# Kernel optimization log

Measured on AMD Instinct MI355X. Metric: run time of the kernel, lower is better.

The kernel has to match this reference:

```python
import jax, jax.numpy as jnp
import numpy as np

B, N, D = 16, 4096, 768   # bags, instances per bag, feature dim
H, L, K = 12, 2, 16       # heads, MHA layers, topk
DH = D // H               # head dim (also gate hidden dim)


def _ln(x, g, b, eps=1e-5):
    m = x.mean(-1, keepdims=True)
    v = x.var(-1, keepdims=True)
    return (x - m) / jnp.sqrt(v + eps) * g + b


def setup_inputs() -> dict:
    key = jax.random.key(0)
    ks = jax.random.split(key, 8)
    s = 0.02
    return {
        "x": jax.random.normal(ks[0], (B, N, D), jnp.float32),
        "cls_token": jax.random.normal(ks[1], (1, 1, D), jnp.float32),
        "ln_g": jnp.ones((D,), jnp.float32),
        "ln_b": jnp.zeros((D,), jnp.float32),
        "gln_g": jnp.ones((D,), jnp.float32),
        "gln_b": jnp.zeros((D,), jnp.float32),
        "gW1": jax.random.normal(ks[2], (DH, D), jnp.float32) * s,
        "gb1": jnp.zeros((DH,), jnp.float32),
        "gW2": jax.random.normal(ks[3], (1, DH), jnp.float32) * s,
        "gb2": jnp.zeros((1,), jnp.float32),
        "Wqkv": jax.random.normal(ks[4], (L, 3 * D, D), jnp.float32) * s,
        "bqkv": jnp.zeros((L, 3 * D), jnp.float32),
        "Wo": jax.random.normal(ks[5], (L, D, D), jnp.float32) * s,
        "bo": jnp.zeros((L, D), jnp.float32),
    }


def reference(x, cls_token, ln_g, ln_b, gln_g, gln_b, gW1, gb1, gW2, gb2, Wqkv, bqkv, Wo, bo):
    # --- per-bag attention gate: LN -> Linear(D,DH) -> GELU -> Linear(DH,1) -> sigmoid ---
    z = _ln(x, gln_g, gln_b)                                      # [B,N,D]
    h = jax.nn.gelu(jnp.einsum('bnd,ed->bne', z, gW1) + gb1, approximate=False)
    w = jax.nn.sigmoid((jnp.einsum('bne,oe->bno', h, gW2) + gb2)[..., 0])  # [B,N]
    # --- top-k selection (argsort descending, take first K) + gather + weight ---
    topv, topi = jax.lax.top_k(w, K)                              # [B,K]
    sel = jnp.take_along_axis(x, topi[..., None], axis=1) * topv[..., None]  # [B,K,D]
    # --- prepend cls token, shared LayerNorm ---
    cls = jnp.broadcast_to(cls_token, (B, 1, D))
    seq = jnp.concatenate([cls, sel], axis=1)                     # [B,K+1,D]
    z0 = _ln(seq, ln_g, ln_b)
    a = z0
    S = K + 1
    scale = 1.0 / jnp.sqrt(jnp.asarray(DH, jnp.float32))
    # --- stacked MHA; residual always from z0, shared ln (matches source) ---
    for l in range(L):
        qkv = jnp.einsum('bsd,ed->bse', a, Wqkv[l]) + bqkv[l]     # [B,S,3D]
        q, k, v = jnp.split(qkv, 3, axis=-1)
        q = q.reshape(B, S, H, DH)
        k = k.reshape(B, S, H, DH)
        v = v.reshape(B, S, H, DH)
        att = jax.nn.softmax(jnp.einsum('bqhd,bkhd->bhqk', q, k) * scale, axis=-1)
        o = jnp.einsum('bhqk,bkhd->bqhd', att, v).reshape(B, S, D)
        o = jnp.einsum('bsd,ed->bse', o, Wo[l]) + bo[l]
        a = _ln(z0 + o, ln_g, ln_b)
    # dropout is identity in eval mode
    return a[:, 0, :]                                             # [B,D]
```

## Files before the change

kernel.cpp:

```cpp
#include <hip/hip_runtime.h>
#include <hip/hip_bf16.h>
#include <hip/hip_cooperative_groups.h>
#include <math.h>

namespace cg = cooperative_groups;

#define B_   16
#define N_   4096
#define D_   768
#define H_   12
#define L_   2
#define K_   16
#define S_   17
#define M_   272
#define BN_  65536
#define GRID_ 256

typedef __bf16 bf16x8 __attribute__((ext_vector_type(8)));
typedef float  f32x4  __attribute__((ext_vector_type(4)));

static __device__ __forceinline__ unsigned short f2bf(float f) {
    __bf16 h = (__bf16)f;
    return __builtin_bit_cast(unsigned short, h);
}
static __device__ __forceinline__ float bf2f(unsigned short u) {
    __bf16 h = __builtin_bit_cast(__bf16, u);
    return (float)h;
}
static __device__ __forceinline__ unsigned long long umax64(unsigned long long a, unsigned long long b) {
    return a > b ? a : b;
}


static __device__ __forceinline__
void gate_block(unsigned short* smem,
                const float* __restrict__ x,  const float* __restrict__ gln_g,
                const float* __restrict__ gln_b, const float* __restrict__ gW1,
                const float* __restrict__ gb1, const float* __restrict__ gW2,
                const float* __restrict__ gb2, float* __restrict__ wbuf,
                int bn0, int t)
{
    char* XhB = (char*)(smem);
    char* XlB = (char*)(smem + 8192);
    char* WhB = (char*)(smem + 16384);
    char* WlB = (char*)(smem + 20480);

    const int trow  = t >> 1;
    const int thalf = (t & 1) * 32;
    const int te    = t >> 2;
    const int tq    = (t & 3) * 16;

    const float* xrow = x + (size_t)(bn0 + trow) * D_ + thalf;
    const float* wrow = gW1 + (size_t)te * D_ + tq;

    const int wv = t >> 6;
    const int la = t & 63;
    const int fr = la & 15;
    const int fq = la >> 4;

    f32x4 acc[2][4];
    #pragma unroll
    for (int mi = 0; mi < 2; ++mi)
        #pragma unroll
        for (int ni = 0; ni < 4; ++ni) {
            f32x4 z = {0.f, 0.f, 0.f, 0.f};
            acc[mi][ni] = z;
        }

    float sxp = 0.f, sxxp = 0.f;
    float a1p = 0.f, a2p = 0.f;

    for (int kt = 0; kt < 12; ++kt) {
        __syncthreads();
        const float* src = xrow + kt * 64;
        #pragma unroll
        for (int j = 0; j < 8; ++j) {
            float4 v = *(const float4*)(src + j * 4);
            sxp  += v.x + v.y + v.z + v.w;
            sxxp += v.x * v.x + v.y * v.y + v.z * v.z + v.w * v.w;
            ushort4 hh, ll;
            hh.x = f2bf(v.x); ll.x = f2bf(v.x - bf2f(hh.x));
            hh.y = f2bf(v.y); ll.y = f2bf(v.y - bf2f(hh.y));
            hh.z = f2bf(v.z); ll.z = f2bf(v.z - bf2f(hh.z));
            hh.w = f2bf(v.w); ll.w = f2bf(v.w - bf2f(hh.w));
            int byte = trow * 128 + (thalf + j * 4) * 2;
            int sw   = byte ^ ((trow & 7) << 4);
            *(ushort4*)(XhB + sw) = hh;
            *(ushort4*)(XlB + sw) = ll;
        }
        const float* wsrc = wrow + kt * 64;
        const float* gsrc = gln_g + kt * 64 + tq;
        const float* bsrc = gln_b + kt * 64 + tq;
        #pragma unroll
        for (int j = 0; j < 4; ++j) {
            float4 w4 = *(const float4*)(wsrc + j * 4);
            float4 g4 = *(const float4*)(gsrc + j * 4);
            float4 b4 = *(const float4*)(bsrc + j * 4);
            float4 wt;
            wt.x = w4.x * g4.x; wt.y = w4.y * g4.y;
            wt.z = w4.z * g4.z; wt.w = w4.w * g4.w;
            a1p += wt.x + wt.y + wt.z + wt.w;
            a2p += b4.x * w4.x + b4.y * w4.y + b4.z * w4.z + b4.w * w4.w;
            ushort4 hh, ll;
            hh.x = f2bf(wt.x); ll.x = f2bf(wt.x - bf2f(hh.x));
            hh.y = f2bf(wt.y); ll.y = f2bf(wt.y - bf2f(hh.y));
            hh.z = f2bf(wt.z); ll.z = f2bf(wt.z - bf2f(hh.z));
            hh.w = f2bf(wt.w); ll.w = f2bf(wt.w - bf2f(hh.w));
            int byte = te * 128 + (tq + j * 4) * 2;
            int sw   = byte ^ ((te & 7) << 4);
            *(ushort4*)(WhB + sw) = hh;
            *(ushort4*)(WlB + sw) = ll;
        }
        __syncthreads();
        #pragma unroll
        for (int ks = 0; ks < 2; ++ks) {
            int k0 = ks * 32 + fq * 8;
            bf16x8 ah[2], al[2], bh[4], bl[4];
            #pragma unroll
            for (int mi = 0; mi < 2; ++mi) {
                int r    = wv * 32 + mi * 16 + fr;
                int byte = (r * 128 + k0 * 2) ^ ((r & 7) << 4);
                ah[mi] = *(const bf16x8*)(XhB + byte);
                al[mi] = *(const bf16x8*)(XlB + byte);
            }
            #pragma unroll
            for (int ni = 0; ni < 4; ++ni) {
                int e    = ni * 16 + fr;
                int byte = (e * 128 + k0 * 2) ^ ((e & 7) << 4);
                bh[ni] = *(const bf16x8*)(WhB + byte);
                bl[ni] = *(const bf16x8*)(WlB + byte);
            }
            #pragma unroll
            for (int mi = 0; mi < 2; ++mi)
                #pragma unroll
                for (int ni = 0; ni < 4; ++ni) {
                    acc[mi][ni] = __builtin_amdgcn_mfma_f32_16x16x32_bf16(ah[mi], bh[ni], acc[mi][ni], 0, 0, 0);
                    acc[mi][ni] = __builtin_amdgcn_mfma_f32_16x16x32_bf16(ah[mi], bl[ni], acc[mi][ni], 0, 0, 0);
                    acc[mi][ni] = __builtin_amdgcn_mfma_f32_16x16x32_bf16(al[mi], bh[ni], acc[mi][ni], 0, 0, 0);
                }
        }
    }
    __syncthreads();

    float* F    = (float*)smem;
    float* mS   = F;
    float* rS   = F + 128;
    float* A1s  = F + 256;
    float* A2s  = F + 320;
    float* redS = F + 384;
    float* redQ = F + 640;
    float* rA1  = F + 896;
    float* rA2  = F + 1152;

    redS[trow * 2 + (t & 1)] = sxp;
    redQ[trow * 2 + (t & 1)] = sxxp;
    rA1[te * 4 + (t & 3)] = a1p;
    rA2[te * 4 + (t & 3)] = a2p;
    __syncthreads();
    if (t < 128) {
        float s = redS[t * 2] + redS[t * 2 + 1];
        float q = redQ[t * 2] + redQ[t * 2 + 1];
        float m = s * (1.0f / D_);
        mS[t] = m;
        rS[t] = rsqrtf(q * (1.0f / D_) - m * m + 1e-5f);
    }
    if (t < 64) {
        A1s[t] = rA1[t * 4] + rA1[t * 4 + 1] + rA1[t * 4 + 2] + rA1[t * 4 + 3];
        A2s[t] = rA2[t * 4] + rA2[t * 4 + 1] + rA2[t * 4 + 2] + rA2[t * 4 + 3];
    }
    __syncthreads();

    float w2v[4], a1v[4], a2b[4];
    #pragma unroll
    for (int ni = 0; ni < 4; ++ni) {
        int e = ni * 16 + fr;
        w2v[ni] = gW2[e];
        a1v[ni] = A1s[e];
        a2b[ni] = A2s[e] + gb1[e];
    }
    float gb2v = gb2[0];

    #pragma unroll
    for (int mi = 0; mi < 2; ++mi) {
        #pragma unroll
        for (int j = 0; j < 4; ++j) {
            int inst = wv * 32 + mi * 16 + fq * 4 + j;
            float m = mS[inst], rs = rS[inst];
            float tp = 0.f;
            #pragma unroll
            for (int ni = 0; ni < 4; ++ni) {
                float h  = rs * (acc[mi][ni][j] - m * a1v[ni]) + a2b[ni];
                float hg = 0.5f * h * (1.0f + erff(h * 0.70710678118654752f));
                tp = fmaf(hg, w2v[ni], tp);
            }
            tp += __shfl_xor(tp, 1);
            tp += __shfl_xor(tp, 2);
            tp += __shfl_xor(tp, 4);
            tp += __shfl_xor(tp, 8);
            if (fr == 0) wbuf[bn0 + inst] = 1.0f / (1.0f + expf(-(tp + gb2v)));
        }
    }
}

static __device__ __forceinline__
void topk_block(unsigned long long* SB, const float* __restrict__ wbuf,
                float* __restrict__ topv, int* __restrict__ topi, int b, int t)
{
    unsigned long long* wred   = SB;
    unsigned long long* winkey = SB + 8;
    const int la = t & 63, wid = t >> 6;

    unsigned long long key[16];
    #pragma unroll
    for (int j = 0; j < 16; ++j) {
        int i = t + 256 * j;
        float v = wbuf[(size_t)b * N_ + i];
        key[j] = ((unsigned long long)__float_as_uint(v) << 12) | (unsigned long long)(4095 - i);
    }
    for (int k = 0; k < K_; ++k) {
        unsigned long long kk = key[0];
        #pragma unroll
        for (int j = 1; j < 16; ++j) kk = umax64(kk, key[j]);
        #pragma unroll
        for (int o = 1; o < 64; o <<= 1) kk = umax64(kk, (unsigned long long)__shfl_xor(kk, o));
        if (la == 0) wred[wid] = kk;
        __syncthreads();
        if (t == 0) {
            unsigned long long m = umax64(umax64(wred[0], wred[1]), umax64(wred[2], wred[3]));
            *winkey = m;
            int wi = 4095 - (int)(m & 0xfffULL);
            topv[b * K_ + k] = __uint_as_float((unsigned int)(m >> 12));
            topi[b * K_ + k] = wi;
        }
        __syncthreads();
        unsigned long long m = *winkey;
        int wi = 4095 - (int)(m & 0xfffULL);
        #pragma unroll
        for (int j = 0; j < 16; ++j)
            if (wi == t + 256 * j) key[j] = 0ULL;
        __syncthreads();
    }
}

static __device__ __forceinline__
void build_row(float* sm, const float* __restrict__ x, const float* __restrict__ cls,
               const float* __restrict__ ln_g, const float* __restrict__ ln_b,
               const float* __restrict__ topv, const int* __restrict__ topi,
               float* __restrict__ z0, float* __restrict__ abuf, int r, int t)
{
    const int b = r / S_, s = r % S_;
    float v[3];
    if (s == 0) {
        #pragma unroll
        for (int p = 0; p < 3; ++p) v[p] = cls[t + 256 * p];
    } else {
        int   idx = topi[b * K_ + s - 1];
        float tv  = topv[b * K_ + s - 1];
        const float* row = &x[((size_t)b * N_ + idx) * D_];
        #pragma unroll
        for (int p = 0; p < 3; ++p) v[p] = row[t + 256 * p] * tv;
    }
    float sum = 0.f, ss = 0.f;
    #pragma unroll
    for (int p = 0; p < 3; ++p) { sum += v[p]; ss += v[p] * v[p]; }
    #pragma unroll
    for (int o = 32; o; o >>= 1) { sum += __shfl_down(sum, o); ss += __shfl_down(ss, o); }
    int wid = t >> 6, la = t & 63;
    if (la == 0) { sm[wid * 2] = sum; sm[wid * 2 + 1] = ss; }
    __syncthreads();
    sum = sm[0] + sm[2] + sm[4] + sm[6];
    ss  = sm[1] + sm[3] + sm[5] + sm[7];
    __syncthreads();
    float m = sum * (1.0f / D_), rstd = rsqrtf(ss * (1.0f / D_) - m * m + 1e-5f);
    #pragma unroll
    for (int p = 0; p < 3; ++p) {
        int d = t + 256 * p;
        float z = (v[p] - m) * rstd * ln_g[d] + ln_b[d];
        z0[(size_t)r * D_ + d]   = z;
        abuf[(size_t)r * D_ + d] = z;
    }
}

static __device__ __forceinline__
void gemm_stage(char* SB, const float* __restrict__ A, const float* __restrict__ W,
                const float* __restrict__ bias, float* __restrict__ C, int N,
                int m0, int n0, int t)
{
    char* AhB = SB;
    char* AlB = SB + 8192;
    char* WhB = SB + 16384;
    char* WlB = SB + 24576;

    const int sr = t >> 2;
    const int sc = (t & 3) * 16;
    const int gm = m0 + sr;
    const bool aok = (gm < M_);
    const float* asrc = A + (size_t)gm * D_ + sc;
    const float* wsrc = W + (size_t)(n0 + sr) * D_ + sc;

    const int wv = t >> 6, la = t & 63;
    const int fr = la & 15, fq = la >> 4;
    const int wm = (wv & 1) * 32, wn = (wv >> 1) * 32;

    f32x4 acc[2][2];
    #pragma unroll
    for (int mi = 0; mi < 2; ++mi)
        #pragma unroll
        for (int ni = 0; ni < 2; ++ni) {
            f32x4 z = {0.f, 0.f, 0.f, 0.f};
            acc[mi][ni] = z;
        }

    float4 pa[4], pw[4];
    #pragma unroll
    for (int q = 0; q < 4; ++q) {
        pa[q] = aok ? *(const float4*)(asrc + q * 4) : make_float4(0.f, 0.f, 0.f, 0.f);
        pw[q] = *(const float4*)(wsrc + q * 4);
    }

    const int abyte0 = sr * 128 + sc * 2;
    const int asw0   = (abyte0)      ^ ((sr & 7) << 4);
    const int asw1   = (abyte0 + 16) ^ ((sr & 7) << 4);

    for (int kt = 0; kt < 12; ++kt) {
        __syncthreads();
        {
            ushort4 hh[4], ll[4];
            #pragma unroll
            for (int q = 0; q < 4; ++q) {
                hh[q].x = f2bf(pa[q].x); ll[q].x = f2bf(pa[q].x - bf2f(hh[q].x));
                hh[q].y = f2bf(pa[q].y); ll[q].y = f2bf(pa[q].y - bf2f(hh[q].y));
                hh[q].z = f2bf(pa[q].z); ll[q].z = f2bf(pa[q].z - bf2f(hh[q].z));
                hh[q].w = f2bf(pa[q].w); ll[q].w = f2bf(pa[q].w - bf2f(hh[q].w));
            }
            *(ushort4*)(AhB + asw0)     = hh[0];
            *(ushort4*)(AhB + asw0 + 8) = hh[1];
            *(ushort4*)(AhB + asw1)     = hh[2];
            *(ushort4*)(AhB + asw1 + 8) = hh[3];
            *(ushort4*)(AlB + asw0)     = ll[0];
            *(ushort4*)(AlB + asw0 + 8) = ll[1];
            *(ushort4*)(AlB + asw1)     = ll[2];
            *(ushort4*)(AlB + asw1 + 8) = ll[3];
            #pragma unroll
            for (int q = 0; q < 4; ++q) {
                hh[q].x = f2bf(pw[q].x); ll[q].x = f2bf(pw[q].x - bf2f(hh[q].x));
                hh[q].y = f2bf(pw[q].y); ll[q].y = f2bf(pw[q].y - bf2f(hh[q].y));
                hh[q].z = f2bf(pw[q].z); ll[q].z = f2bf(pw[q].z - bf2f(hh[q].z));
                hh[q].w = f2bf(pw[q].w); ll[q].w = f2bf(pw[q].w - bf2f(hh[q].w));
            }
            *(ushort4*)(WhB + asw0)     = hh[0];
            *(ushort4*)(WhB + asw0 + 8) = hh[1];
            *(ushort4*)(WhB + asw1)     = hh[2];
            *(ushort4*)(WhB + asw1 + 8) = hh[3];
            *(ushort4*)(WlB + asw0)     = ll[0];
            *(ushort4*)(WlB + asw0 + 8) = ll[1];
            *(ushort4*)(WlB + asw1)     = ll[2];
            *(ushort4*)(WlB + asw1 + 8) = ll[3];
        }
        __syncthreads();
        if (kt < 11) {
            const float* an  = asrc + (kt + 1) * 64;
            const float* wn2 = wsrc + (kt + 1) * 64;
            #pragma unroll
            for (int q = 0; q < 4; ++q) {
                pa[q] = aok ? *(const float4*)(an + q * 4) : make_float4(0.f, 0.f, 0.f, 0.f);
                pw[q] = *(const float4*)(wn2 + q * 4);
            }
        }
        #pragma unroll
        for (int ks = 0; ks < 2; ++ks) {
            int kb = ks * 64 + fq * 16;
            bf16x8 ah[2], al[2], bh[2], bl[2];
            #pragma unroll
            for (int mi = 0; mi < 2; ++mi) {
                int r    = wm + mi * 16 + fr;
                int byte = (r * 128 + kb) ^ ((r & 7) << 4);
                ah[mi] = *(const bf16x8*)(AhB + byte);
                al[mi] = *(const bf16x8*)(AlB + byte);
            }
            #pragma unroll
            for (int ni = 0; ni < 2; ++ni) {
                int r    = wn + ni * 16 + fr;
                int byte = (r * 128 + kb) ^ ((r & 7) << 4);
                bh[ni] = *(const bf16x8*)(WhB + byte);
                bl[ni] = *(const bf16x8*)(WlB + byte);
            }
            #pragma unroll
            for (int mi = 0; mi < 2; ++mi)
                #pragma unroll
                for (int ni = 0; ni < 2; ++ni) {
                    acc[mi][ni] = __builtin_amdgcn_mfma_f32_16x16x32_bf16(ah[mi], bh[ni], acc[mi][ni], 0, 0, 0);
                    acc[mi][ni] = __builtin_amdgcn_mfma_f32_16x16x32_bf16(ah[mi], bl[ni], acc[mi][ni], 0, 0, 0);
                    acc[mi][ni] = __builtin_amdgcn_mfma_f32_16x16x32_bf16(al[mi], bh[ni], acc[mi][ni], 0, 0, 0);
                }
        }
    }

    #pragma unroll
    for (int mi = 0; mi < 2; ++mi) {
        #pragma unroll
        for (int j = 0; j < 4; ++j) {
            int m = m0 + wm + mi * 16 + fq * 4 + j;
            if (m < M_) {
                #pragma unroll
                for (int ni = 0; ni < 2; ++ni) {
                    int n = n0 + wn + ni * 16 + fr;
                    C[(size_t)m * N + n] = acc[mi][ni][j] + bias[n];
                }
            }
        }
    }
}

static __device__ __forceinline__
void attn_block(float* F, const float* __restrict__ qkvb, float* __restrict__ obuf,
                int bh, int t)
{
    float* qs  = F;
    float* ks  = F + S_ * 65;
    float* vs  = F + 2 * S_ * 65;
    float* att = F + 3 * S_ * 65;
    const int b = bh / H_, h = bh % H_;
    const int bq = b * S_;
    for (int idx = t; idx < S_ * 64; idx += 256) {
        int s = idx >> 6, d = idx & 63;
        size_t off = (size_t)(bq + s) * (3 * D_) + h * 64 + d;
        qs[s * 65 + d] = qkvb[off];
        ks[s * 65 + d] = qkvb[off + D_];
        vs[s * 65 + d] = qkvb[off + 2 * D_];
    }
    __syncthreads();
    for (int idx = t; idx < S_ * S_; idx += 256) {
        int i = idx / S_, j = idx % S_;
        float sdot = 0.f;
        #pragma unroll
        for (int d = 0; d < 64; ++d) sdot = fmaf(qs[i * 65 + d], ks[j * 65 + d], sdot);
        att[i * 18 + j] = sdot * 0.125f;
    }
    __syncthreads();
    if (t < S_) {
        float mx = -1e30f;
        for (int j = 0; j < S_; ++j) mx = fmaxf(mx, att[t * 18 + j]);
        float ssum = 0.f;
        for (int j = 0; j < S_; ++j) { float e = expf(att[t * 18 + j] - mx); att[t * 18 + j] = e; ssum += e; }
        float inv = 1.0f / ssum;
        for (int j = 0; j < S_; ++j) att[t * 18 + j] *= inv;
    }
    __syncthreads();
    for (int idx = t; idx < S_ * 64; idx += 256) {
        int i = idx >> 6, d = idx & 63;
        float s = 0.f;
        #pragma unroll
        for (int j = 0; j < S_; ++j) s = fmaf(att[i * 18 + j], vs[j * 65 + d], s);
        obuf[(size_t)(bq + i) * D_ + h * 64 + d] = s;
    }
}

static __device__ __forceinline__
void resln_row(float* sm, const float* __restrict__ z0, const float* __restrict__ projb,
               const float* __restrict__ ln_g, const float* __restrict__ ln_b,
               float* __restrict__ abuf, float* __restrict__ out, int r, int t, int writeOut)
{
    float v[3];
    #pragma unroll
    for (int p = 0; p < 3; ++p) {
        int d = t + 256 * p;
        v[p] = z0[(size_t)r * D_ + d] + projb[(size_t)r * D_ + d];
    }
    float sum = 0.f, ss = 0.f;
    #pragma unroll
    for (int p = 0; p < 3; ++p) { sum += v[p]; ss += v[p] * v[p]; }
    #pragma unroll
    for (int o = 32; o; o >>= 1) { sum += __shfl_down(sum, o); ss += __shfl_down(ss, o); }
    int wid = t >> 6, la = t & 63;
    if (la == 0) { sm[wid * 2] = sum; sm[wid * 2 + 1] = ss; }
    __syncthreads();
    sum = sm[0] + sm[2] + sm[4] + sm[6];
    ss  = sm[1] + sm[3] + sm[5] + sm[7];
    __syncthreads();
    float m = sum * (1.0f / D_), rstd = rsqrtf(ss * (1.0f / D_) - m * m + 1e-5f);
    #pragma unroll
    for (int p = 0; p < 3; ++p) {
        int d = t + 256 * p;
        float a = (v[p] - m) * rstd * ln_g[d] + ln_b[d];
        abuf[(size_t)r * D_ + d] = a;
        if (writeOut && (r % S_) == 0) out[(size_t)(r / S_) * D_ + d] = a;
    }
}

__global__ __launch_bounds__(256)
void fused_kernel(const float* __restrict__ x, const float* __restrict__ cls,
                  const float* __restrict__ ln_g, const float* __restrict__ ln_b,
                  const float* __restrict__ gln_g, const float* __restrict__ gln_b,
                  const float* __restrict__ gW1, const float* __restrict__ gb1,
                  const float* __restrict__ gW2, const float* __restrict__ gb2,
                  const float* __restrict__ Wqkv, const float* __restrict__ bqkv,
                  const float* __restrict__ Wo, const float* __restrict__ bo,
                  float* out,
                  float* wbuf, float* topv, int* topi,
                  float* z0, float* abuf, float* qkvb, float* obuf, float* projb)
{
    cg::grid_group grid = cg::this_grid();
    __shared__ __align__(16) char SMEM[49152];
    const int bid = blockIdx.x;
    const int t   = threadIdx.x;

    #pragma unroll 1
    for (int half = 0; half < 2; ++half)
        gate_block((unsigned short*)SMEM, x, gln_g, gln_b, gW1, gb1, gW2, gb2,
                   wbuf, bid * 256 + half * 128, t);
    grid.sync();

    if (bid < B_) topk_block((unsigned long long*)SMEM, wbuf, topv, topi, bid, t);
    grid.sync();

    #pragma unroll 1
    for (int r = bid; r < M_; r += GRID_)
        build_row((float*)SMEM, x, cls, ln_g, ln_b, topv, topi, z0, abuf, r, t);
    grid.sync();

    #pragma unroll 1
    for (int l = 0; l < L_; ++l) {
        if (bid < 180)
            gemm_stage(SMEM, abuf, Wqkv + (size_t)l * 3 * D_ * D_,
                       bqkv + (size_t)l * 3 * D_, qkvb, 3 * D_,
                       (bid / 36) * 64, (bid % 36) * 64, t);
        grid.sync();

        if (bid < B_ * H_) attn_block((float*)SMEM, qkvb, obuf, bid, t);
        grid.sync();

        if (bid < 60)
            gemm_stage(SMEM, obuf, Wo + (size_t)l * D_ * D_,
                       bo + (size_t)l * D_, projb, D_,
                       (bid / 12) * 64, (bid % 12) * 64, t);
        grid.sync();

        #pragma unroll 1
        for (int r = bid; r < M_; r += GRID_)
            resln_row((float*)SMEM, z0, projb, ln_g, ln_b, abuf, out, r, t,
                      (l == L_ - 1) ? 1 : 0);
        if (l == 0) grid.sync();
    }
}

__global__ __launch_bounds__(256)
void gate_kernel(const float* __restrict__ x, const float* __restrict__ gln_g,
                 const float* __restrict__ gln_b, const float* __restrict__ gW1,
                 const float* __restrict__ gb1, const float* __restrict__ gW2,
                 const float* __restrict__ gb2, float* __restrict__ wbuf)
{
    __shared__ __align__(16) unsigned short smem[24576];
    gate_block(smem, x, gln_g, gln_b, gW1, gb1, gW2, gb2, wbuf,
               blockIdx.x * 128, threadIdx.x);
}

__global__ __launch_bounds__(256)
void topk_kernel(const float* __restrict__ wbuf, float* __restrict__ topv,
                 int* __restrict__ topi)
{
    __shared__ unsigned long long SB[16];
    topk_block(SB, wbuf, topv, topi, blockIdx.x, threadIdx.x);
}

__global__ __launch_bounds__(256)
void build_kernel(const float* __restrict__ x, const float* __restrict__ cls,
                  const float* __restrict__ ln_g, const float* __restrict__ ln_b,
                  const float* __restrict__ topv, const int* __restrict__ topi,
                  float* __restrict__ z0, float* __restrict__ abuf)
{
    __shared__ float sm[8];
    build_row(sm, x, cls, ln_g, ln_b, topv, topi, z0, abuf, blockIdx.x, threadIdx.x);
}

__global__ __launch_bounds__(256)
void gemm_mfma(const float* __restrict__ A, const float* __restrict__ W,
               const float* __restrict__ bias, float* __restrict__ C, int N)
{
    __shared__ __align__(16) char SB[32768];
    gemm_stage(SB, A, W, bias, C, N, blockIdx.x * 64, blockIdx.y * 64, threadIdx.x);
}

__global__ __launch_bounds__(256)
void attn_kernel(const float* __restrict__ qkvb, float* __restrict__ obuf)
{
    __shared__ __align__(16) float F[3 * S_ * 65 + S_ * 18];
    attn_block(F, qkvb, obuf, blockIdx.x, threadIdx.x);
}

__global__ __launch_bounds__(256)
void resln_kernel(const float* __restrict__ z0, const float* __restrict__ projb,
                  const float* __restrict__ ln_g, const float* __restrict__ ln_b,
                  float* __restrict__ abuf, float* __restrict__ out, int writeOut)
{
    __shared__ float sm[8];
    resln_row(sm, z0, projb, ln_g, ln_b, abuf, out, blockIdx.x, threadIdx.x, writeOut);
}

extern "C" void kernel_launch(void* const* d_in, const int* in_sizes, int n_in,
                              void* d_out, int out_size, void* d_ws, size_t ws_size,
                              hipStream_t stream)
{
    const float* x     = (const float*)d_in[0];
    const float* cls   = (const float*)d_in[1];
    const float* ln_g  = (const float*)d_in[2];
    const float* ln_b  = (const float*)d_in[3];
    const float* gln_g = (const float*)d_in[4];
    const float* gln_b = (const float*)d_in[5];
    const float* gW1   = (const float*)d_in[6];
    const float* gb1   = (const float*)d_in[7];
    const float* gW2   = (const float*)d_in[8];
    const float* gb2   = (const float*)d_in[9];
    const float* Wqkv  = (const float*)d_in[10];
    const float* bqkv  = (const float*)d_in[11];
    const float* Wo    = (const float*)d_in[12];
    const float* bo    = (const float*)d_in[13];
    float* out = (float*)d_out;

    float* ws   = (float*)d_ws;
    float* wbuf = ws;
    float* topv = ws + BN_;
    int*   topi = (int*)(ws + BN_ + 256);
    float* z0   = ws + BN_ + 512;
    float* abuf = z0 + (size_t)M_ * D_;
    float* qkvb = abuf + (size_t)M_ * D_;
    float* obuf = qkvb + (size_t)M_ * 3 * D_;
    float* projb = obuf + (size_t)M_ * D_;

    hipError_t lerr = hipErrorUnknown;
    int nb = 0;
    if (hipOccupancyMaxActiveBlocksPerMultiprocessor(
            &nb, (const void*)fused_kernel, 256, 0) == hipSuccess && nb >= 1) {
        void* args[] = {
            (void*)&x, (void*)&cls, (void*)&ln_g, (void*)&ln_b,
            (void*)&gln_g, (void*)&gln_b, (void*)&gW1, (void*)&gb1,
            (void*)&gW2, (void*)&gb2, (void*)&Wqkv, (void*)&bqkv,
            (void*)&Wo, (void*)&bo, (void*)&out,
            (void*)&wbuf, (void*)&topv, (void*)&topi,
            (void*)&z0, (void*)&abuf, (void*)&qkvb, (void*)&obuf, (void*)&projb
        };
        lerr = hipLaunchCooperativeKernel((const void*)fused_kernel, dim3(GRID_),
                                          dim3(256), args, 0, stream);
    }
    if (lerr != hipSuccess) {
        gate_kernel<<<BN_ / 128, 256, 0, stream>>>(x, gln_g, gln_b, gW1, gb1, gW2, gb2, wbuf);
        topk_kernel<<<B_, 256, 0, stream>>>(wbuf, topv, topi);
        build_kernel<<<M_, 256, 0, stream>>>(x, cls, ln_g, ln_b, topv, topi, z0, abuf);
        for (int l = 0; l < L_; ++l) {
            gemm_mfma<<<dim3(5, 36), 256, 0, stream>>>(abuf, Wqkv + (size_t)l * 3 * D_ * D_,
                                                       bqkv + (size_t)l * 3 * D_, qkvb, 3 * D_);
            attn_kernel<<<B_ * H_, 256, 0, stream>>>(qkvb, obuf);
            gemm_mfma<<<dim3(5, 12), 256, 0, stream>>>(obuf, Wo + (size_t)l * D_ * D_,
                                                       bo + (size_t)l * D_, projb, D_);
            resln_kernel<<<M_, 256, 0, stream>>>(z0, projb, ln_g, ln_b, abuf, out,
                                                 (l == L_ - 1) ? 1 : 0);
        }
    }
}
```

Baseline: 180.4 us.

## Replace cooperative grid kernel with fused per-stage launches and per-head QKV+attention

Drops the cooperative single-kernel design with grid-wide syncs and goes back to separate kernel launches. Top-k is merged with row building, and each head's QKV projection is fused with its attention so the qkv buffer never goes to global memory. The final layer's LN runs only on the cls rows. This removes grid.sync overhead and some intermediate traffic, but adds launch overhead and recomputes A-tile splits once per head.

```diff
diff --git a/kernel.cpp b/kernel.cpp
--- a/kernel.cpp
+++ b/kernel.cpp
@@ -1,9 +1,6 @@
 #include <hip/hip_runtime.h>
 #include <hip/hip_bf16.h>
-#include <hip/hip_cooperative_groups.h>
 #include <math.h>
-
-namespace cg = cooperative_groups;
 
 #define B_   16
 #define N_   4096
@@ -14,7 +11,6 @@
 #define S_   17
 #define M_   272
 #define BN_  65536
-#define GRID_ 256
 
 typedef __bf16 bf16x8 __attribute__((ext_vector_type(8)));
 typedef float  f32x4  __attribute__((ext_vector_type(4)));
@@ -30,20 +26,27 @@
 static __device__ __forceinline__ unsigned long long umax64(unsigned long long a, unsigned long long b) {
     return a > b ? a : b;
 }
-
-
-static __device__ __forceinline__
-void gate_block(unsigned short* smem,
-                const float* __restrict__ x,  const float* __restrict__ gln_g,
-                const float* __restrict__ gln_b, const float* __restrict__ gW1,
-                const float* __restrict__ gb1, const float* __restrict__ gW2,
-                const float* __restrict__ gb2, float* __restrict__ wbuf,
-                int bn0, int t)
+static __device__ __forceinline__ void split4(const float4& v, ushort4& hh, ushort4& ll) {
+    hh.x = f2bf(v.x); ll.x = f2bf(v.x - bf2f(hh.x));
+    hh.y = f2bf(v.y); ll.y = f2bf(v.y - bf2f(hh.y));
+    hh.z = f2bf(v.z); ll.z = f2bf(v.z - bf2f(hh.z));
+    hh.w = f2bf(v.w); ll.w = f2bf(v.w - bf2f(hh.w));
+}
+
+__global__ __launch_bounds__(256)
+void gate_kernel(const float* __restrict__ x, const float* __restrict__ gln_g,
+                 const float* __restrict__ gln_b, const float* __restrict__ gW1,
+                 const float* __restrict__ gb1, const float* __restrict__ gW2,
+                 const float* __restrict__ gb2, float* __restrict__ wbuf)
 {
+    __shared__ __align__(16) unsigned short smem[24576];
     char* XhB = (char*)(smem);
     char* XlB = (char*)(smem + 8192);
     char* WhB = (char*)(smem + 16384);
     char* WlB = (char*)(smem + 20480);
+
+    const int t   = threadIdx.x;
+    const int bn0 = blockIdx.x * 128;
 
     const int trow  = t >> 1;
     const int thalf = (t & 1) * 32;
@@ -79,10 +82,7 @@
             sxp  += v.x + v.y + v.z + v.w;
             sxxp += v.x * v.x + v.y * v.y + v.z * v.z + v.w * v.w;
             ushort4 hh, ll;
-            hh.x = f2bf(v.x); ll.x = f2bf(v.x - bf2f(hh.x));
-            hh.y = f2bf(v.y); ll.y = f2bf(v.y - bf2f(hh.y));
-            hh.z = f2bf(v.z); ll.z = f2bf(v.z - bf2f(hh.z));
-            hh.w = f2bf(v.w); ll.w = f2bf(v.w - bf2f(hh.w));
+            split4(v, hh, ll);
             int byte = trow * 128 + (thalf + j * 4) * 2;
             int sw   = byte ^ ((trow & 7) << 4);
             *(ushort4*)(XhB + sw) = hh;
@@ -102,10 +102,7 @@
             a1p += wt.x + wt.y + wt.z + wt.w;
             a2p += b4.x * w4.x + b4.y * w4.y + b4.z * w4.z + b4.w * w4.w;
             ushort4 hh, ll;
-            hh.x = f2bf(wt.x); ll.x = f2bf(wt.x - bf2f(hh.x));
-            hh.y = f2bf(wt.y); ll.y = f2bf(wt.y - bf2f(hh.y));
-            hh.z = f2bf(wt.z); ll.z = f2bf(wt.z - bf2f(hh.z));
-            hh.w = f2bf(wt.w); ll.w = f2bf(wt.w - bf2f(hh.w));
+            split4(wt, hh, ll);
             int byte = te * 128 + (tq + j * 4) * 2;
             int sw   = byte ^ ((te & 7) << 4);
             *(ushort4*)(WhB + sw) = hh;
@@ -202,12 +199,14 @@
     }
 }
 
-static __device__ __forceinline__
-void topk_block(unsigned long long* SB, const float* __restrict__ wbuf,
-                float* __restrict__ topv, int* __restrict__ topi, int b, int t)
+__global__ __launch_bounds__(256)
+void topkbuild_kernel(const float* __restrict__ x, const float* __restrict__ cls,
+                      const float* __restrict__ ln_g, const float* __restrict__ ln_b,
+                      const float* __restrict__ wbuf, float* __restrict__ z0)
 {
-    unsigned long long* wred   = SB;
-    unsigned long long* winkey = SB + 8;
+    __shared__ unsigned long long SB[40];
+    __shared__ float sm[8];
+    const int b = blockIdx.x, t = threadIdx.x;
     const int la = t & 63, wid = t >> 6;
 
     unsigned long long key[16];
@@ -223,73 +222,199 @@
         for (int j = 1; j < 16; ++j) kk = umax64(kk, key[j]);
         #pragma unroll
         for (int o = 1; o < 64; o <<= 1) kk = umax64(kk, (unsigned long long)__shfl_xor(kk, o));
-        if (la == 0) wred[wid] = kk;
+        if (la == 0) SB[wid] = kk;
         __syncthreads();
         if (t == 0) {
-            unsigned long long m = umax64(umax64(wred[0], wred[1]), umax64(wred[2], wred[3]));
-            *winkey = m;
-            int wi = 4095 - (int)(m & 0xfffULL);
-            topv[b * K_ + k] = __uint_as_float((unsigned int)(m >> 12));
-            topi[b * K_ + k] = wi;
-        }
-        __syncthreads();
-        unsigned long long m = *winkey;
+            unsigned long long m = umax64(umax64(SB[0], SB[1]), umax64(SB[2], SB[3]));
+            SB[8] = m;
+            SB[16 + k] = m;
+        }
+        __syncthreads();
+        unsigned long long m = SB[8];
         int wi = 4095 - (int)(m & 0xfffULL);
         #pragma unroll
         for (int j = 0; j < 16; ++j)
             if (wi == t + 256 * j) key[j] = 0ULL;
         __syncthreads();
     }
-}
-
-static __device__ __forceinline__
-void build_row(float* sm, const float* __restrict__ x, const float* __restrict__ cls,
-               const float* __restrict__ ln_g, const float* __restrict__ ln_b,
-               const float* __restrict__ topv, const int* __restrict__ topi,
-               float* __restrict__ z0, float* __restrict__ abuf, int r, int t)
+
+    for (int s = 0; s < S_; ++s) {
+        float v[3];
+        if (s == 0) {
+            #pragma unroll
+            for (int p = 0; p < 3; ++p) v[p] = cls[t + 256 * p];
+        } else {
+            unsigned long long m = SB[16 + s - 1];
+            int   idx = 4095 - (int)(m & 0xfffULL);
+            float tv  = __uint_as_float((unsigned int)(m >> 12));
+            const float* row = &x[((size_t)b * N_ + idx) * D_];
+            #pragma unroll
+            for (int p = 0; p < 3; ++p) v[p] = row[t + 256 * p] * tv;
+        }
+        float sum = 0.f, ss = 0.f;
+        #pragma unroll
+        for (int p = 0; p < 3; ++p) { sum += v[p]; ss += v[p] * v[p]; }
+        #pragma unroll
+        for (int o = 32; o; o >>= 1) { sum += __shfl_down(sum, o); ss += __shfl_down(ss, o); }
+        if (la == 0) { sm[wid * 2] = sum; sm[wid * 2 + 1] = ss; }
+        __syncthreads();
+        sum = sm[0] + sm[2] + sm[4] + sm[6];
+        ss  = sm[1] + sm[3] + sm[5] + sm[7];
+        __syncthreads();
+        float m = sum * (1.0f / D_), rstd = rsqrtf(ss * (1.0f / D_) - m * m + 1e-5f);
+        #pragma unroll
+        for (int p = 0; p < 3; ++p) {
+            int d = t + 256 * p;
+            z0[((size_t)(b * S_ + s)) * D_ + d] = (v[p] - m) * rstd * ln_g[d] + ln_b[d];
+        }
+    }
+}
+
+__global__ __launch_bounds__(256)
+void qkvattn_kernel(const float* __restrict__ A, const float* __restrict__ Wq,
+                    const float* __restrict__ bq, float* __restrict__ obuf)
 {
-    const int b = r / S_, s = r % S_;
-    float v[3];
-    if (s == 0) {
-        #pragma unroll
-        for (int p = 0; p < 3; ++p) v[p] = cls[t + 256 * p];
-    } else {
-        int   idx = topi[b * K_ + s - 1];
-        float tv  = topv[b * K_ + s - 1];
-        const float* row = &x[((size_t)b * N_ + idx) * D_];
-        #pragma unroll
-        for (int p = 0; p < 3; ++p) v[p] = row[t + 256 * p] * tv;
-    }
-    float sum = 0.f, ss = 0.f;
-    #pragma unroll
-    for (int p = 0; p < 3; ++p) { sum += v[p]; ss += v[p] * v[p]; }
-    #pragma unroll
-    for (int o = 32; o; o >>= 1) { sum += __shfl_down(sum, o); ss += __shfl_down(ss, o); }
-    int wid = t >> 6, la = t & 63;
-    if (la == 0) { sm[wid * 2] = sum; sm[wid * 2 + 1] = ss; }
-    __syncthreads();
-    sum = sm[0] + sm[2] + sm[4] + sm[6];
-    ss  = sm[1] + sm[3] + sm[5] + sm[7];
-    __syncthreads();
-    float m = sum * (1.0f / D_), rstd = rsqrtf(ss * (1.0f / D_) - m * m + 1e-5f);
-    #pragma unroll
-    for (int p = 0; p < 3; ++p) {
-        int d = t + 256 * p;
-        float z = (v[p] - m) * rstd * ln_g[d] + ln_b[d];
-        z0[(size_t)r * D_ + d]   = z;
-        abuf[(size_t)r * D_ + d] = z;
-    }
-}
-
-static __device__ __forceinline__
-void gemm_stage(char* SB, const float* __restrict__ A, const float* __restrict__ W,
-                const float* __restrict__ bias, float* __restrict__ C, int N,
-                int m0, int n0, int t)
+    __shared__ __align__(16) char SMEM[57344];
+    char* AhB = SMEM;
+    char* AlB = SMEM + 4096;
+    char* WhB = SMEM + 8192;
+    char* WlB = SMEM + 32768;
+
+    const int bid = blockIdx.x, b = bid / H_, h = bid % H_;
+    const int t = threadIdx.x;
+    const int wv = t >> 6, la = t & 63, fr = la & 15, fq = la >> 4;
+
+    const int ar  = t >> 3;
+    const int ac  = (t & 7) * 8;
+    const int wr4 = t >> 2;
+    const int wc  = (t & 3) * 16;
+
+    f32x4 acc[2][3];
+    #pragma unroll
+    for (int mi = 0; mi < 2; ++mi)
+        #pragma unroll
+        for (int ni = 0; ni < 3; ++ni) {
+            f32x4 z = {0.f, 0.f, 0.f, 0.f};
+            acc[mi][ni] = z;
+        }
+
+    for (int kt = 0; kt < 12; ++kt) {
+        __syncthreads();
+        #pragma unroll
+        for (int q2 = 0; q2 < 2; ++q2) {
+            ushort4 hh = {0, 0, 0, 0}, ll = {0, 0, 0, 0};
+            if (ar < S_) {
+                float4 v = *(const float4*)(A + ((size_t)(b * S_ + ar)) * D_ + kt * 64 + ac + q2 * 4);
+                split4(v, hh, ll);
+            }
+            int byte = (ar * 128 + (ac + q2 * 4) * 2) ^ ((ar & 7) << 4);
+            *(ushort4*)(AhB + byte) = hh;
+            *(ushort4*)(AlB + byte) = ll;
+        }
+        #pragma unroll
+        for (int jj = 0; jj < 3; ++jj) {
+            int wr   = jj * 64 + wr4;
+            int grow = (wr >> 6) * D_ + h * 64 + (wr & 63);
+            const float* wsrc = Wq + (size_t)grow * D_ + kt * 64 + wc;
+            #pragma unroll
+            for (int q4 = 0; q4 < 4; ++q4) {
+                float4 w = *(const float4*)(wsrc + q4 * 4);
+                ushort4 hh, ll;
+                split4(w, hh, ll);
+                int byte = (wr * 128 + (wc + q4 * 4) * 2) ^ ((wr & 7) << 4);
+                *(ushort4*)(WhB + byte) = hh;
+                *(ushort4*)(WlB + byte) = ll;
+            }
+        }
+        __syncthreads();
+        #pragma unroll
+        for (int ks = 0; ks < 2; ++ks) {
+            int kb = ks * 64 + fq * 16;
+            bf16x8 ah[2], al[2], bh[3], bl[3];
+            #pragma unroll
+            for (int mi = 0; mi < 2; ++mi) {
+                int r    = mi * 16 + fr;
+                int byte = (r * 128 + kb) ^ ((r & 7) << 4);
+                ah[mi] = *(const bf16x8*)(AhB + byte);
+                al[mi] = *(const bf16x8*)(AlB + byte);
+            }
+            #pragma unroll
+            for (int ni = 0; ni < 3; ++ni) {
+                int r    = (wv * 3 + ni) * 16 + fr;
+                int byte = (r * 128 + kb) ^ ((r & 7) << 4);
+                bh[ni] = *(const bf16x8*)(WhB + byte);
+                bl[ni] = *(const bf16x8*)(WlB + byte);
+            }
+            #pragma unroll
+            for (int mi = 0; mi < 2; ++mi)
+                #pragma unroll
+                for (int ni = 0; ni < 3; ++ni) {
+                    acc[mi][ni] = __builtin_amdgcn_mfma_f32_16x16x32_bf16(ah[mi], bh[ni], acc[mi][ni], 0, 0, 0);
+                    acc[mi][ni] = __builtin_amdgcn_mfma_f32_16x16x32_bf16(ah[mi], bl[ni], acc[mi][ni], 0, 0, 0);
+                    acc[mi][ni] = __builtin_amdgcn_mfma_f32_16x16x32_bf16(al[mi], bh[ni], acc[mi][ni], 0, 0, 0);
+                }
+        }
+    }
+    __syncthreads();
+
+    float* QKV = (float*)SMEM;
+    float* att = (float*)(SMEM + S_ * 200 * 4);
+
+    #pragma unroll
+    for (int mi = 0; mi < 2; ++mi)
+        #pragma unroll
+        for (int j = 0; j < 4; ++j) {
+            int row = mi * 16 + fq * 4 + j;
+            if (row < S_) {
+                #pragma unroll
+                for (int ni = 0; ni < 3; ++ni) {
+                    int col  = (wv * 3 + ni) * 16 + fr;
+                    int grow = (col >> 6) * D_ + h * 64 + (col & 63);
+                    QKV[row * 200 + col] = acc[mi][ni][j] + bq[grow];
+                }
+            }
+        }
+    __syncthreads();
+
+    for (int idx = t; idx < S_ * S_; idx += 256) {
+        int i = idx / S_, j = idx % S_;
+        float sdot = 0.f;
+        #pragma unroll
+        for (int d = 0; d < 64; ++d)
+            sdot = fmaf(QKV[i * 200 + d], QKV[j * 200 + 64 + d], sdot);
+        att[i * 18 + j] = sdot * 0.125f;
+    }
+    __syncthreads();
+    if (t < S_) {
+        float mx = -1e30f;
+        for (int j = 0; j < S_; ++j) mx = fmaxf(mx, att[t * 18 + j]);
+        float ssum = 0.f;
+        for (int j = 0; j < S_; ++j) { float e = expf(att[t * 18 + j] - mx); att[t * 18 + j] = e; ssum += e; }
+        float inv = 1.0f / ssum;
+        for (int j = 0; j < S_; ++j) att[t * 18 + j] *= inv;
+    }
+    __syncthreads();
+    for (int idx = t; idx < S_ * 64; idx += 256) {
+        int i = idx >> 6, d = idx & 63;
+        float s = 0.f;
+        #pragma unroll
+        for (int j = 0; j < S_; ++j) s = fmaf(att[i * 18 + j], QKV[j * 200 + 128 + d], s);
+        obuf[((size_t)(b * S_ + i)) * D_ + h * 64 + d] = s;
+    }
+}
+
+__global__ __launch_bounds__(256)
+void gemm_mfma(const float* __restrict__ A, const float* __restrict__ W,
+               const float* __restrict__ bias, float* __restrict__ C, int N)
 {
+    __shared__ __align__(16) char SB[32768];
     char* AhB = SB;
     char* AlB = SB + 8192;
     char* WhB = SB + 16384;
     char* WlB = SB + 24576;
+
+    const int t  = threadIdx.x;
+    const int m0 = blockIdx.x * 64, n0 = blockIdx.y * 64;
 
     const int sr = t >> 2;
     const int sc = (t & 3) * 16;
@@ -327,12 +452,7 @@
         {
             ushort4 hh[4], ll[4];
             #pragma unroll
-            for (int q = 0; q < 4; ++q) {
-                hh[q].x = f2bf(pa[q].x); ll[q].x = f2bf(pa[q].x - bf2f(hh[q].x));
-                hh[q].y = f2bf(pa[q].y); ll[q].y = f2bf(pa[q].y - bf2f(hh[q].y));
-                hh[q].z = f2bf(pa[q].z); ll[q].z = f2bf(pa[q].z - bf2f(hh[q].z));
-                hh[q].w = f2bf(pa[q].w); ll[q].w = f2bf(pa[q].w - bf2f(hh[q].w));
-            }
+            for (int q = 0; q < 4; ++q) split4(pa[q], hh[q], ll[q]);
             *(ushort4*)(AhB + asw0)     = hh[0];
             *(ushort4*)(AhB + asw0 + 8) = hh[1];
             *(ushort4*)(AhB + asw1)     = hh[2];
@@ -342,12 +462,7 @@
             *(ushort4*)(AlB + asw1)     = ll[2];
             *(ushort4*)(AlB + asw1 + 8) = ll[3];
             #pragma unroll
-            for (int q = 0; q < 4; ++q) {
-                hh[q].x = f2bf(pw[q].x); ll[q].x = f2bf(pw[q].x - bf2f(hh[q].x));
-                hh[q].y = f2bf(pw[q].y); ll[q].y = f2bf(pw[q].y - bf2f(hh[q].y));
-                hh[q].z = f2bf(pw[q].z); ll[q].z = f2bf(pw[q].z - bf2f(hh[q].z));
-                hh[q].w = f2bf(pw[q].w); ll[q].w = f2bf(pw[q].w - bf2f(hh[q].w));
-            }
+            for (int q = 0; q < 4; ++q) split4(pw[q], hh[q], ll[q]);
             *(ushort4*)(WhB + asw0)     = hh[0];
             *(ushort4*)(WhB + asw0 + 8) = hh[1];
             *(ushort4*)(WhB + asw1)     = hh[2];
@@ -412,55 +527,13 @@
     }
 }
 
-static __device__ __forceinline__
-void attn_block(float* F, const float* __restrict__ qkvb, float* __restrict__ obuf,
-                int bh, int t)
+__global__ __launch_bounds__(256)
+void resln_kernel(const float* __restrict__ z0, const float* __restrict__ projb,
+                  const float* __restrict__ ln_g, const float* __restrict__ ln_b,
+                  float* __restrict__ abuf)
 {
-    float* qs  = F;
-    float* ks  = F + S_ * 65;
-    float* vs  = F + 2 * S_ * 65;
-    float* att = F + 3 * S_ * 65;
-    const int b = bh / H_, h = bh % H_;
-    const int bq = b * S_;
-    for (int idx = t; idx < S_ * 64; idx += 256) {
-        int s = idx >> 6, d = idx & 63;
-        size_t off = (size_t)(bq + s) * (3 * D_) + h * 64 + d;
-        qs[s * 65 + d] = qkvb[off];
-        ks[s * 65 + d] = qkvb[off + D_];
-        vs[s * 65 + d] = qkvb[off + 2 * D_];
-    }
-    __syncthreads();
-    for (int idx = t; idx < S_ * S_; idx += 256) {
-        int i = idx / S_, j = idx % S_;
-        float sdot = 0.f;
-        #pragma unroll
-        for (int d = 0; d < 64; ++d) sdot = fmaf(qs[i * 65 + d], ks[j * 65 + d], sdot);
-        att[i * 18 + j] = sdot * 0.125f;
-    }
-    __syncthreads();
-    if (t < S_) {
-        float mx = -1e30f;
-        for (int j = 0; j < S_; ++j) mx = fmaxf(mx, att[t * 18 + j]);
-        float ssum = 0.f;
-        for (int j = 0; j < S_; ++j) { float e = expf(att[t * 18 + j] - mx); att[t * 18 + j] = e; ssum += e; }
-        float inv = 1.0f / ssum;
-        for (int j = 0; j < S_; ++j) att[t * 18 + j] *= inv;
-    }
-    __syncthreads();
-    for (int idx = t; idx < S_ * 64; idx += 256) {
-        int i = idx >> 6, d = idx & 63;
-        float s = 0.f;
-        #pragma unroll
-        for (int j = 0; j < S_; ++j) s = fmaf(att[i * 18 + j], vs[j * 65 + d], s);
-        obuf[(size_t)(bq + i) * D_ + h * 64 + d] = s;
-    }
-}
-
-static __device__ __forceinline__
-void resln_row(float* sm, const float* __restrict__ z0, const float* __restrict__ projb,
-               const float* __restrict__ ln_g, const float* __restrict__ ln_b,
-               float* __restrict__ abuf, float* __restrict__ out, int r, int t, int writeOut)
-{
+    __shared__ float sm[8];
+    const int r = blockIdx.x, t = threadIdx.x;
     float v[3];
     #pragma unroll
     for (int p = 0; p < 3; ++p) {
@@ -477,124 +550,44 @@
     __syncthreads();
     sum = sm[0] + sm[2] + sm[4] + sm[6];
     ss  = sm[1] + sm[3] + sm[5] + sm[7];
-    __syncthreads();
     float m = sum * (1.0f / D_), rstd = rsqrtf(ss * (1.0f / D_) - m * m + 1e-5f);
     #pragma unroll
     for (int p = 0; p < 3; ++p) {
         int d = t + 256 * p;
-        float a = (v[p] - m) * rstd * ln_g[d] + ln_b[d];
-        abuf[(size_t)r * D_ + d] = a;
-        if (writeOut && (r % S_) == 0) out[(size_t)(r / S_) * D_ + d] = a;
+        abuf[(size_t)r * D_ + d] = (v[p] - m) * rstd * ln_g[d] + ln_b[d];
     }
 }
 
 __global__ __launch_bounds__(256)
-void fused_kernel(const float* __restrict__ x, const float* __restrict__ cls,
+void outln_kernel(const float* __restrict__ z0, const float* __restrict__ projb,
                   const float* __restrict__ ln_g, const float* __restrict__ ln_b,
-                  const float* __restrict__ gln_g, const float* __restrict__ gln_b,
-                  const float* __restrict__ gW1, const float* __restrict__ gb1,
-                  const float* __restrict__ gW2, const float* __restrict__ gb2,
-                  const float* __restrict__ Wqkv, const float* __restrict__ bqkv,
-                  const float* __restrict__ Wo, const float* __restrict__ bo,
-                  float* out,
-                  float* wbuf, float* topv, int* topi,
-                  float* z0, float* abuf, float* qkvb, float* obuf, float* projb)
-{
-    cg::grid_group grid = cg::this_grid();
-    __shared__ __align__(16) char SMEM[49152];
-    const int bid = blockIdx.x;
-    const int t   = threadIdx.x;
-
-    #pragma unroll 1
-    for (int half = 0; half < 2; ++half)
-        gate_block((unsigned short*)SMEM, x, gln_g, gln_b, gW1, gb1, gW2, gb2,
-                   wbuf, bid * 256 + half * 128, t);
-    grid.sync();
-
-    if (bid < B_) topk_block((unsigned long long*)SMEM, wbuf, topv, topi, bid, t);
-    grid.sync();
-
-    #pragma unroll 1
-    for (int r = bid; r < M_; r += GRID_)
-        build_row((float*)SMEM, x, cls, ln_g, ln_b, topv, topi, z0, abuf, r, t);
-    grid.sync();
-
-    #pragma unroll 1
-    for (int l = 0; l < L_; ++l) {
-        if (bid < 180)
-            gemm_stage(SMEM, abuf, Wqkv + (size_t)l * 3 * D_ * D_,
-                       bqkv + (size_t)l * 3 * D_, qkvb, 3 * D_,
-                       (bid / 36) * 64, (bid % 36) * 64, t);
-        grid.sync();
-
-        if (bid < B_ * H_) attn_block((float*)SMEM, qkvb, obuf, bid, t);
-        grid.sync();
-
-        if (bid < 60)
-            gemm_stage(SMEM, obuf, Wo + (size_t)l * D_ * D_,
-                       bo + (size_t)l * D_, projb, D_,
-                       (bid / 12) * 64, (bid % 12) * 64, t);
-        grid.sync();
-
-        #pragma unroll 1
-        for (int r = bid; r < M_; r += GRID_)
-            resln_row((float*)SMEM, z0, projb, ln_g, ln_b, abuf, out, r, t,
-                      (l == L_ - 1) ? 1 : 0);
-        if (l == 0) grid.sync();
-    }
-}
-
-__global__ __launch_bounds__(256)
-void gate_kernel(const float* __restrict__ x, const float* __restrict__ gln_g,
-                 const float* __restrict__ gln_b, const float* __restrict__ gW1,
-                 const float* __restrict__ gb1, const float* __restrict__ gW2,
-                 const float* __restrict__ gb2, float* __restrict__ wbuf)
-{
-    __shared__ __align__(16) unsigned short smem[24576];
-    gate_block(smem, x, gln_g, gln_b, gW1, gb1, gW2, gb2, wbuf,
-               blockIdx.x * 128, threadIdx.x);
-}
-
-__global__ __launch_bounds__(256)
-void topk_kernel(const float* __restrict__ wbuf, float* __restrict__ topv,
-                 int* __restrict__ topi)
-{
-    __shared__ unsigned long long SB[16];
-    topk_block(SB, wbuf, topv, topi, blockIdx.x, threadIdx.x);
-}
-
-__global__ __launch_bounds__(256)
-void build_kernel(const float* __restrict__ x, const float* __restrict__ cls,
-                  const float* __restrict__ ln_g, const float* __restrict__ ln_b,
-                  const float* __restrict__ topv, const int* __restrict__ topi,
-                  float* __restrict__ z0, float* __restrict__ abuf)
+                  float* __restrict__ out)
 {
     __shared__ float sm[8];
-    build_row(sm, x, cls, ln_g, ln_b, topv, topi, z0, abuf, blockIdx.x, threadIdx.x);
-}
-
-__global__ __launch_bounds__(256)
-void gemm_mfma(const float* __restrict__ A, const float* __restrict__ W,
-               const float* __restrict__ bias, float* __restrict__ C, int N)
-{
-    __shared__ __align__(16) char SB[32768];
-    gemm_stage(SB, A, W, bias, C, N, blockIdx.x * 64, blockIdx.y * 64, threadIdx.x);
-}
-
-__global__ __launch_bounds__(256)
-void attn_kernel(const float* __restrict__ qkvb, float* __restrict__ obuf)
-{
-    __shared__ __align__(16) float F[3 * S_ * 65 + S_ * 18];
-    attn_block(F, qkvb, obuf, blockIdx.x, threadIdx.x);
-}
-
-__global__ __launch_bounds__(256)
-void resln_kernel(const float* __restrict__ z0, const float* __restrict__ projb,
-                  const float* __restrict__ ln_g, const float* __restrict__ ln_b,
-                  float* __restrict__ abuf, float* __restrict__ out, int writeOut)
-{
-    __shared__ float sm[8];
-    resln_row(sm, z0, projb, ln_g, ln_b, abuf, out, blockIdx.x, threadIdx.x, writeOut);
+    const int b = blockIdx.x, t = threadIdx.x;
+    const size_t r = (size_t)b * S_;
+    float v[3];
+    #pragma unroll
+    for (int p = 0; p < 3; ++p) {
+        int d = t + 256 * p;
+        v[p] = z0[r * D_ + d] + projb[r * D_ + d];
+    }
+    float sum = 0.f, ss = 0.f;
+    #pragma unroll
+    for (int p = 0; p < 3; ++p) { sum += v[p]; ss += v[p] * v[p]; }
+    #pragma unroll
+    for (int o = 32; o; o >>= 1) { sum += __shfl_down(sum, o); ss += __shfl_down(ss, o); }
+    int wid = t >> 6, la = t & 63;
+    if (la == 0) { sm[wid * 2] = sum; sm[wid * 2 + 1] = ss; }
+    __syncthreads();
+    sum = sm[0] + sm[2] + sm[4] + sm[6];
+    ss  = sm[1] + sm[3] + sm[5] + sm[7];
+    float m = sum * (1.0f / D_), rstd = rsqrtf(ss * (1.0f / D_) - m * m + 1e-5f);
+    #pragma unroll
+    for (int p = 0; p < 3; ++p) {
+        int d = t + 256 * p;
+        out[(size_t)b * D_ + d] = (v[p] - m) * rstd * ln_g[d] + ln_b[d];
+    }
 }
 
 extern "C" void kernel_launch(void* const* d_in, const int* in_sizes, int n_in,
@@ -617,43 +610,22 @@
     const float* bo    = (const float*)d_in[13];
     float* out = (float*)d_out;
 
-    float* ws   = (float*)d_ws;
-    float* wbuf = ws;
-    float* topv = ws + BN_;
-    int*   topi = (int*)(ws + BN_ + 256);
-    float* z0   = ws + BN_ + 512;
-    float* abuf = z0 + (size_t)M_ * D_;
-    float* qkvb = abuf + (size_t)M_ * D_;
-    float* obuf = qkvb + (size_t)M_ * 3 * D_;
+    float* ws    = (float*)d_ws;
+    float* wbuf  = ws;
+    float* z0    = ws + BN_;
+    float* abuf  = z0 + (size_t)M_ * D_;
+    float* obuf  = abuf + (size_t)M_ * D_;
     float* projb = obuf + (size_t)M_ * D_;
 
-    hipError_t lerr = hipErrorUnknown;
-    int nb = 0;
-    if (hipOccupancyMaxActiveBlocksPerMultiprocessor(
-            &nb, (const void*)fused_kernel, 256, 0) == hipSuccess && nb >= 1) {
-        void* args[] = {
-            (void*)&x, (void*)&cls, (void*)&ln_g, (void*)&ln_b,
-            (void*)&gln_g, (void*)&gln_b, (void*)&gW1, (void*)&gb1,
-            (void*)&gW2, (void*)&gb2, (void*)&Wqkv, (void*)&bqkv,
-            (void*)&Wo, (void*)&bo, (void*)&out,
-            (void*)&wbuf, (void*)&topv, (void*)&topi,
-            (void*)&z0, (void*)&abuf, (void*)&qkvb, (void*)&obuf, (void*)&projb
-        };
-        lerr = hipLaunchCooperativeKernel((const void*)fused_kernel, dim3(GRID_),
-                                          dim3(256), args, 0, stream);
-    }
-    if (lerr != hipSuccess) {
-        gate_kernel<<<BN_ / 128, 256, 0, stream>>>(x, gln_g, gln_b, gW1, gb1, gW2, gb2, wbuf);
-        topk_kernel<<<B_, 256, 0, stream>>>(wbuf, topv, topi);
-        build_kernel<<<M_, 256, 0, stream>>>(x, cls, ln_g, ln_b, topv, topi, z0, abuf);
-        for (int l = 0; l < L_; ++l) {
-            gemm_mfma<<<dim3(5, 36), 256, 0, stream>>>(abuf, Wqkv + (size_t)l * 3 * D_ * D_,
-                                                       bqkv + (size_t)l * 3 * D_, qkvb, 3 * D_);
-            attn_kernel<<<B_ * H_, 256, 0, stream>>>(qkvb, obuf);
-            gemm_mfma<<<dim3(5, 12), 256, 0, stream>>>(obuf, Wo + (size_t)l * D_ * D_,
-                                                       bo + (size_t)l * D_, projb, D_);
-            resln_kernel<<<M_, 256, 0, stream>>>(z0, projb, ln_g, ln_b, abuf, out,
-                                                 (l == L_ - 1) ? 1 : 0);
-        }
-    }
-}
+    gate_kernel<<<BN_ / 128, 256, 0, stream>>>(x, gln_g, gln_b, gW1, gb1, gW2, gb2, wbuf);
+    topkbuild_kernel<<<B_, 256, 0, stream>>>(x, cls, ln_g, ln_b, wbuf, z0);
+
+    qkvattn_kernel<<<B_ * H_, 256, 0, stream>>>(z0, Wqkv, bqkv, obuf);
+    gemm_mfma<<<dim3(5, 12), 256, 0, stream>>>(obuf, Wo, bo, projb, D_);
+    resln_kernel<<<M_, 256, 0, stream>>>(z0, projb, ln_g, ln_b, abuf);
+
+    qkvattn_kernel<<<B_ * H_, 256, 0, stream>>>(abuf, Wqkv + (size_t)3 * D_ * D_,
+                                                bqkv + 3 * D_, obuf);
+    gemm_mfma<<<dim3(5, 12), 256, 0, stream>>>(obuf, Wo + (size_t)D_ * D_, bo + D_, projb, D_);
+    outln_kernel<<<B_, 256, 0, stream>>>(z0, projb, ln_g, ln_b, out);
+}
```

Result: slower. 192.7 us (+6.8%).
